# Performance work log

Hardware: AMD Instinct MI355X
Metric: run time of the kernel (lower is better)

Reference implementation:

```python
import jax, jax.numpy as jnp
import numpy as np

DIM = 1024
HEADS = 16
HEAD_DIM = DIM // HEADS
THETA = 10000.0


def _freqs_cis(d, n, theta=THETA):
    # complex rotary frequencies, shape (n, d//2)
    pos = jnp.arange(n, dtype=jnp.float32)
    inv = 1.0 / theta ** (jnp.arange(0, d, 2, dtype=jnp.float32) / d)
    ang = jnp.outer(pos, inv)
    return jax.lax.complex(jnp.cos(ang), jnp.sin(ang))


def _to_complex(x):
    # (..., d) -> (..., d//2) complex via adjacent pairs
    xr = x.astype(jnp.float32).reshape(*x.shape[:-1], -1, 2)
    return jax.lax.complex(xr[..., 0], xr[..., 1])


def _to_real(xc):
    # (..., d//2) complex -> (..., d) interleaved real/imag
    return jnp.stack([jnp.real(xc), jnp.imag(xc)], axis=-1).reshape(*xc.shape[:-1], -1)


def setup_inputs() -> dict:
    key = jax.random.key(0)
    k1, k2, k3 = jax.random.split(key, 3)
    b, seq = 2, 2048
    x = jax.random.normal(k1, (b, DIM, seq), dtype=jnp.float32)
    w_qkv = jax.random.normal(k2, (3 * DIM, DIM), dtype=jnp.float32) * (DIM ** -0.5)
    w_out = jax.random.normal(k3, (DIM, DIM), dtype=jnp.float32) * (DIM ** -0.5)
    return {"x": x, "w_qkv": w_qkv, "w_out": w_out}


def reference(x, w_qkv, w_out):
    b, dim, n = x.shape
    h, hd = HEADS, HEAD_DIM
    scale = hd ** -0.5
    xt = jnp.swapaxes(x, -1, -2)                      # (b, t, dim)
    qkv = jnp.einsum('btd,ed->bte', xt, w_qkv)        # (b, t, 3*dim)
    q, k, v = jnp.split(qkv, 3, axis=-1)
    q = q.reshape(b, n, h, hd)
    k = k.reshape(b, n, h, hd)
    v = v.reshape(b, n, h, hd)
    # rotary embedding on q, k
    fc = _freqs_cis(hd, n)[None, :, None, :]          # (1, t, 1, hd//2)
    q = _to_real(_to_complex(q) * fc).astype(x.dtype)
    k = _to_real(_to_complex(k) * fc).astype(x.dtype)
    # naive full attention
    logits = jnp.einsum('bqhd,bkhd->bhqk', q, k) * scale
    probs = jax.nn.softmax(logits, axis=-1)
    out = jnp.einsum('bhqk,bkhd->bqhd', probs, v)     # (b, t, h, hd)
    out = out.reshape(b, n, dim)
    out = jnp.einsum('btd,ed->bte', out, w_out)       # (b, t, dim)
    return jnp.swapaxes(out, -1, -2)                  # (b, dim, t)
```

## Files before the change

kernel.cpp:

```cpp
#include <hip/hip_runtime.h>
#include <hip/hip_bf16.h>
#include <math.h>

#define B 2
#define N 2048
#define D 1024
#define H 16
#define HD 64

typedef __attribute__((ext_vector_type(8))) short short8;
typedef __attribute__((ext_vector_type(4))) float f32x4;
typedef __attribute__((ext_vector_type(16))) float f32x16;
typedef __attribute__((ext_vector_type(4))) unsigned short ush4;
typedef __attribute__((ext_vector_type(4))) unsigned int uint4v;

__device__ __forceinline__ float bf2f(unsigned short u) {
  unsigned int x = ((unsigned int)u) << 16;
  float f;
  __builtin_memcpy(&f, &x, 4);
  return f;
}
__device__ __forceinline__ unsigned short f2bf(float f) {
  unsigned int x;
  __builtin_memcpy(&x, &f, 4);
  x = x + 0x7fffu + ((x >> 16) & 1u);
  return (unsigned short)(x >> 16);
}
__device__ __forceinline__ unsigned int pk2(float lo, float hi) {
  union { __hip_bfloat162 h; unsigned int u; } cv;
  cv.h = __float22bfloat162_rn(make_float2(lo, hi));
  return cv.u;
}
__device__ __forceinline__ short8 mk_frag(unsigned int w0, unsigned int w1,
                                          unsigned int w2, unsigned int w3) {
  union { uint4v u; short8 s; } cv;
  cv.u = (uint4v){w0, w1, w2, w3};
  return cv.s;
}

__device__ __forceinline__ void gload16(const unsigned short* g, unsigned short* l) {
  __builtin_amdgcn_global_load_lds(
      (const __attribute__((address_space(1))) unsigned int*)(const void*)g,
      (__attribute__((address_space(3))) unsigned int*)(void*)l, 16, 0, 0);
}

__global__ void prep_k(const float* __restrict__ wqkv, unsigned short* __restrict__ wqkv_bf,
                       const float* __restrict__ wout, unsigned short* __restrict__ wout_bf,
                       float2* __restrict__ tab) {
  int blk = blockIdx.x;
  if (blk < 4096) {
    const float* src = (blk < 3072) ? wqkv : wout;
    unsigned short* dst = (blk < 3072) ? wqkv_bf : wout_bf;
    int i = (blk < 3072 ? blk : blk - 3072) * 256 + threadIdx.x;
    float4 v = ((const float4*)src)[i];
    ush4 o;
    o[0] = f2bf(v.x); o[1] = f2bf(v.y); o[2] = f2bf(v.z); o[3] = f2bf(v.w);
    *(ush4*)&dst[i * 4] = o;
  } else {
    int idx = (blk - 4096) * 256 + threadIdx.x;
    int t = idx >> 5, p = idx & 31;
    float inv = powf(10000.f, -(float)p / 32.f);
    float ang = (float)t * inv;
    float s, c;
    sincosf(ang, &s, &c);
    tab[idx] = make_float2(c, s);
  }
}

__global__ __launch_bounds__(256) void transpose_x(const float* __restrict__ x,
                                                   unsigned short* __restrict__ xt) {
  __shared__ float tile[32][33];
  const int tx = threadIdx.x, ty = threadIdx.y;
  const int t0 = blockIdx.x * 32, d0 = blockIdx.y * 32, bb = blockIdx.z;
#pragma unroll
  for (int i = 0; i < 4; ++i) {
    int r = ty * 4 + i;
    tile[r][tx] = x[(size_t)bb * D * N + (size_t)(d0 + r) * N + t0 + tx];
  }
  __syncthreads();
#pragma unroll
  for (int i = 0; i < 4; ++i) {
    int r = ty * 4 + i;
    xt[((size_t)(bb * N) + t0 + r) * D + d0 + tx] = f2bf(tile[tx][r]);
  }
}

template <int MODE>
__global__ __launch_bounds__(256) void gemm_bt(const unsigned short* __restrict__ A,
                                               const unsigned short* __restrict__ Bt,
                                               float* __restrict__ outf,
                                               unsigned short* __restrict__ qkbuf,
                                               unsigned short* __restrict__ vtbuf) {
  __shared__ unsigned short Asm[128 * 64];
  __shared__ unsigned short Bsm[128 * 64];
  const int tid = threadIdx.x;
  const int lane = tid & 63, wid = tid >> 6;
  const int ln = lane & 15, lh = lane >> 4;
  const int wr = wid >> 1, wc = wid & 1;
  const int m0 = blockIdx.x * 128, n0 = blockIdx.y * 128;

  f32x4 acc[4][4];
#pragma unroll
  for (int i = 0; i < 4; ++i)
#pragma unroll
    for (int j = 0; j < 4; ++j) acc[i][j] = (f32x4){0.f, 0.f, 0.f, 0.f};

  for (int k0 = 0; k0 < 1024; k0 += 64) {
#pragma unroll
    for (int jj = 0; jj < 4; ++jj) {
      int slot = tid + jj * 256;
      int row = slot >> 3, u = slot & 7;
      int usw = (u ^ (row & 7)) * 8;
      gload16(&A[(size_t)(m0 + row) * 1024 + k0 + usw], &Asm[slot * 8]);
    }
#pragma unroll
    for (int jj = 0; jj < 4; ++jj) {
      int slot = tid + jj * 256;
      int row = slot >> 3, u = slot & 7;
      int usw = (u ^ (row & 7)) * 8;
      gload16(&Bt[(size_t)(n0 + row) * 1024 + k0 + usw], &Bsm[slot * 8]);
    }
    __syncthreads();
#pragma unroll
    for (int s = 0; s < 2; ++s) {
      short8 af[4], bfr[4];
#pragma unroll
      for (int i = 0; i < 4; ++i) {
        int row = wr * 64 + i * 16 + ln;
        int u = ((s * 4 + lh) ^ (row & 7)) * 8;
        af[i] = *(const short8*)&Asm[row * 64 + u];
      }
#pragma unroll
      for (int j = 0; j < 4; ++j) {
        int row = wc * 64 + j * 16 + ln;
        int u = ((s * 4 + lh) ^ (row & 7)) * 8;
        bfr[j] = *(const short8*)&Bsm[row * 64 + u];
      }
#pragma unroll
      for (int i = 0; i < 4; ++i)
#pragma unroll
        for (int j = 0; j < 4; ++j)
          acc[i][j] = __builtin_amdgcn_mfma_f32_16x16x32_bf16(af[i], bfr[j], acc[i][j], 0, 0, 0);
    }
    __syncthreads();
  }

#pragma unroll
  for (int i = 0; i < 4; ++i) {
    int mrow = m0 + wr * 64 + i * 16 + lh * 4;
    int bb = mrow >> 11, t = mrow & 2047;
#pragma unroll
    for (int j = 0; j < 4; ++j) {
      int e = n0 + wc * 64 + j * 16 + ln;
      if (MODE == 1) {
        float* op = outf + (size_t)bb * D * N + (size_t)e * N + t;
        *(f32x4*)op = acc[i][j];
      } else {
        if (e < 2048) {
#pragma unroll
          for (int jj = 0; jj < 4; ++jj)
            qkbuf[((size_t)(bb * N + t + jj)) * 2048 + e] = f2bf(acc[i][j][jj]);
        } else {
          ush4 v;
#pragma unroll
          for (int jj = 0; jj < 4; ++jj) v[jj] = f2bf(acc[i][j][jj]);
          *(ush4*)&vtbuf[((size_t)bb * 1024 + (e - 2048)) * N + t] = v;
        }
      }
    }
  }
}

__global__ void rope_kernel(unsigned short* __restrict__ qk, const float2* __restrict__ tab) {
  int idx = blockIdx.x * 256 + threadIdx.x;
  int e = (idx & 255) * 8;
  int t = (idx >> 8) & 2047;
  int bb = idx >> 19;
  int p0 = (e & 63) >> 1;
  const float qscl = 0.125f * 1.4426950408889634f;
  float sc = (e < 1024) ? qscl : 1.0f;
  unsigned short* p = qk + ((size_t)(bb * N + t)) * 2048 + e;
  short8 v = *(short8*)p;
#pragma unroll
  for (int q = 0; q < 4; ++q) {
    float2 cs = tab[t * 32 + p0 + q];
    float xe = bf2f((unsigned short)v[2 * q]);
    float xo = bf2f((unsigned short)v[2 * q + 1]);
    v[2 * q] = (short)f2bf((xe * cs.x - xo * cs.y) * sc);
    v[2 * q + 1] = (short)f2bf((xe * cs.y + xo * cs.x) * sc);
  }
  *(short8*)p = v;
}

__global__ __launch_bounds__(512, 4) void attn_kernel(const unsigned short* __restrict__ qk,
                                                      const unsigned short* __restrict__ vt,
                                                      unsigned short* __restrict__ ob) {
  __shared__ __align__(16) char smem[66048];
  const int tid = threadIdx.x;
  const int lane = tid & 63, wid = tid >> 6;
  const int l31 = lane & 31, hi = lane >> 5;
  const int g = wid >> 2, wl = wid & 3;
  const int tidg = tid & 255;
  const int L = blockIdx.x;
  const int hh = L & 31, qb = L >> 5;
  const int bb = hh >> 4, h = hh & 15;
  const unsigned short* Qg = qk + (size_t)bb * N * 2048 + h * 64;
  const unsigned short* Kg = Qg + 1024;
  const unsigned short* Vg = vt + ((size_t)bb * 1024 + h * 64) * N;

  unsigned short* Ksm[2] = {(unsigned short*)smem + (g * 2 + 0) * 4096,
                            (unsigned short*)smem + (g * 2 + 1) * 4096};
  unsigned short* Vsm[2] = {(unsigned short*)(smem + 32768) + (g * 2 + 0) * 4096,
                            (unsigned short*)(smem + 32768) + (g * 2 + 1) * 4096};

  const int q = qb * 128 + wl * 32 + l31;
  short8 qf[4];
#pragma unroll
  for (int c = 0; c < 4; ++c)
    qf[c] = *(const short8*)&Qg[(size_t)q * 2048 + c * 16 + hi * 8];

  f32x16 oL, oH;
#pragma unroll
  for (int r = 0; r < 16; ++r) { oL[r] = 0.f; oH[r] = 0.f; }
  float lrun = 0.f;

  const int kb0 = g * 1024;
  auto STAGE = [&](int buf, int kb) {
#pragma unroll
    for (int jj = 0; jj < 2; ++jj) {
      int slot = tidg + jj * 256;
      int row = slot >> 3, u = slot & 7;
      int usw = (u ^ (row & 7)) * 8;
      gload16(&Kg[(size_t)(kb + row) * 2048 + usw], &Ksm[buf][slot * 8]);
    }
#pragma unroll
    for (int jj = 0; jj < 2; ++jj) {
      int slot = tidg + jj * 256;
      int row = slot >> 3, u = slot & 7;
      int usw = (u ^ (row & 7)) * 8;
      gload16(&Vg[(size_t)row * N + kb + usw], &Vsm[buf][slot * 8]);
    }
  };

  STAGE(0, kb0);
  __syncthreads();
  int cur = 0;
  for (int t = 0; t < 16; ++t) {
    if (t < 15) STAGE(cur ^ 1, kb0 + (t + 1) * 64);
    f32x16 s0, s1;
#pragma unroll
    for (int r = 0; r < 16; ++r) { s0[r] = 0.f; s1[r] = 0.f; }
    __builtin_amdgcn_s_setprio(1);
#pragma unroll
    for (int c = 0; c < 4; ++c) {
      short8 ka = *(const short8*)&Ksm[cur][l31 * 64 + (((c * 2 + hi) ^ (l31 & 7)) * 8)];
      s0 = __builtin_amdgcn_mfma_f32_32x32x16_bf16(ka, qf[c], s0, 0, 0, 0);
      int r1 = 32 + l31;
      short8 kb2 = *(const short8*)&Ksm[cur][r1 * 64 + (((c * 2 + hi) ^ (r1 & 7)) * 8)];
      s1 = __builtin_amdgcn_mfma_f32_32x32x16_bf16(kb2, qf[c], s1, 0, 0, 0);
    }
    __builtin_amdgcn_s_setprio(0);
    float lsum = 0.f;
#pragma unroll
    for (int r = 0; r < 16; ++r) {
      s0[r] = __builtin_amdgcn_exp2f(s0[r]);
      s1[r] = __builtin_amdgcn_exp2f(s1[r]);
      lsum += s0[r] + s1[r];
    }
    lrun += lsum;
    unsigned int W[16];
#pragma unroll
    for (int i = 0; i < 8; ++i) {
      W[i] = pk2(s0[2 * i], s0[2 * i + 1]);
      W[8 + i] = pk2(s1[2 * i], s1[2 * i + 1]);
    }
    short8 pf[4];
#pragma unroll
    for (int c = 0; c < 4; ++c) {
      unsigned int a0 = W[4 * c + 0], b0 = W[4 * c + 2];
      unsigned int a1 = W[4 * c + 1], b1 = W[4 * c + 3];
      asm volatile("v_permlane32_swap_b32 %0, %1" : "+v"(a0), "+v"(b0));
      asm volatile("v_permlane32_swap_b32 %0, %1" : "+v"(a1), "+v"(b1));
      pf[c] = mk_frag(a0, a1, b0, b1);
    }
    __builtin_amdgcn_s_setprio(1);
#pragma unroll
    for (int c = 0; c < 4; ++c) {
      short8 va = *(const short8*)&Vsm[cur][l31 * 64 + (((c * 2 + hi) ^ (l31 & 7)) * 8)];
      oL = __builtin_amdgcn_mfma_f32_32x32x16_bf16(va, pf[c], oL, 0, 0, 0);
      int rH = 32 + l31;
      short8 vb = *(const short8*)&Vsm[cur][rH * 64 + (((c * 2 + hi) ^ (rH & 7)) * 8)];
      oH = __builtin_amdgcn_mfma_f32_32x32x16_bf16(vb, pf[c], oH, 0, 0, 0);
    }
    __builtin_amdgcn_s_setprio(0);
    __syncthreads();
    cur ^= 1;
  }
  lrun += __shfl_xor(lrun, 32, 64);

  __syncthreads();
  float* cmb = (float*)smem;
  float* lbuf = (float*)(smem + 65536);
  const int ql = wl * 32 + l31;
  if (g) {
#pragma unroll
    for (int r4 = 0; r4 < 4; ++r4) {
      int bo = (ql * 256 + r4 * 32 + hi * 16) ^ ((ql & 7) << 4);
      *(f32x4*)((char*)cmb + bo) =
          (f32x4){oL[r4 * 4], oL[r4 * 4 + 1], oL[r4 * 4 + 2], oL[r4 * 4 + 3]};
      int bo2 = (ql * 256 + 128 + r4 * 32 + hi * 16) ^ ((ql & 7) << 4);
      *(f32x4*)((char*)cmb + bo2) =
          (f32x4){oH[r4 * 4], oH[r4 * 4 + 1], oH[r4 * 4 + 2], oH[r4 * 4 + 3]};
    }
    if (!hi) lbuf[ql] = lrun;
  }
  __syncthreads();
  if (!g) {
#pragma unroll
    for (int r4 = 0; r4 < 4; ++r4) {
      int bo = (ql * 256 + r4 * 32 + hi * 16) ^ ((ql & 7) << 4);
      f32x4 pL = *(const f32x4*)((const char*)cmb + bo);
      int bo2 = (ql * 256 + 128 + r4 * 32 + hi * 16) ^ ((ql & 7) << 4);
      f32x4 pH = *(const f32x4*)((const char*)cmb + bo2);
#pragma unroll
      for (int i = 0; i < 4; ++i) {
        oL[r4 * 4 + i] += pL[i];
        oH[r4 * 4 + i] += pH[i];
      }
    }
    lrun += lbuf[ql];
    float inv = 1.f / lrun;
    unsigned short* obp = ob + ((size_t)(bb * N + q)) * 1024 + h * 64;
#pragma unroll
    for (int r4 = 0; r4 < 4; ++r4) {
      ush4 vL, vH;
#pragma unroll
      for (int i = 0; i < 4; ++i) {
        vL[i] = f2bf(oL[r4 * 4 + i] * inv);
        vH[i] = f2bf(oH[r4 * 4 + i] * inv);
      }
      *(ush4*)&obp[r4 * 8 + hi * 4] = vL;
      *(ush4*)&obp[32 + r4 * 8 + hi * 4] = vH;
    }
  }
}

extern "C" void kernel_launch(void* const* d_in, const int* in_sizes, int n_in,
                              void* d_out, int out_size, void* d_ws, size_t ws_size,
                              hipStream_t stream) {
  const float* x = (const float*)d_in[0];
  const float* w_qkv = (const float*)d_in[1];
  const float* w_out = (const float*)d_in[2];
  float* out = (float*)d_out;
  char* ws = (char*)d_ws;

  unsigned short* wqkv_bf = (unsigned short*)ws;
  unsigned short* wout_bf = (unsigned short*)(ws + 6291456);
  unsigned short* xt      = (unsigned short*)(ws + 8388608);
  unsigned short* qkbuf   = (unsigned short*)(ws + 16777216);
  unsigned short* vtbuf   = (unsigned short*)(ws + 33554432);
  float2* tab             = (float2*)(ws + 41943040);

  prep_k<<<4352, 256, 0, stream>>>(w_qkv, wqkv_bf, w_out, wout_bf, tab);
  transpose_x<<<dim3(N / 32, D / 32, B), dim3(32, 8), 0, stream>>>(x, xt);

  gemm_bt<0><<<dim3(32, 24), 256, 0, stream>>>(xt, wqkv_bf, nullptr, qkbuf, vtbuf);
  rope_kernel<<<4096, 256, 0, stream>>>(qkbuf, tab);
  attn_kernel<<<512, 512, 0, stream>>>(qkbuf, vtbuf, xt );
  gemm_bt<1><<<dim3(32, 8), 256, 0, stream>>>(xt, wout_bf, out, nullptr, nullptr);
}
```

Before: 133.4 us.

## Split Q/K buffers, store Q transposed, stage K/V through registers

```diff
diff --git a/kernel.cpp b/kernel.cpp
--- a/kernel.cpp
+++ b/kernel.cpp
@@ -46,7 +46,7 @@
 
 __global__ void prep_k(const float* __restrict__ wqkv, unsigned short* __restrict__ wqkv_bf,
                        const float* __restrict__ wout, unsigned short* __restrict__ wout_bf,
-                       float2* __restrict__ tab) {
+                       float2* __restrict__ tab, float2* __restrict__ tabT) {
   int blk = blockIdx.x;
   if (blk < 4096) {
     const float* src = (blk < 3072) ? wqkv : wout;
@@ -64,6 +64,7 @@
     float s, c;
     sincosf(ang, &s, &c);
     tab[idx] = make_float2(c, s);
+    tabT[p * 2048 + t] = make_float2(c, s);
   }
 }
 
@@ -89,7 +90,8 @@
 __global__ __launch_bounds__(256) void gemm_bt(const unsigned short* __restrict__ A,
                                                const unsigned short* __restrict__ Bt,
                                                float* __restrict__ outf,
-                                               unsigned short* __restrict__ qkbuf,
+                                               unsigned short* __restrict__ q_em,
+                                               unsigned short* __restrict__ kbuf,
                                                unsigned short* __restrict__ vtbuf) {
   __shared__ unsigned short Asm[128 * 64];
   __shared__ unsigned short Bsm[128 * 64];
@@ -156,14 +158,16 @@
         float* op = outf + (size_t)bb * D * N + (size_t)e * N + t;
         *(f32x4*)op = acc[i][j];
       } else {
-        if (e < 2048) {
+        ush4 v;
+#pragma unroll
+        for (int jj = 0; jj < 4; ++jj) v[jj] = f2bf(acc[i][j][jj]);
+        if (e < 1024) {
+          *(ush4*)&q_em[((size_t)bb * 1024 + e) * N + t] = v;
+        } else if (e < 2048) {
 #pragma unroll
           for (int jj = 0; jj < 4; ++jj)
-            qkbuf[((size_t)(bb * N + t + jj)) * 2048 + e] = f2bf(acc[i][j][jj]);
+            kbuf[((size_t)(bb * N + t + jj)) * 1024 + (e - 1024)] = v[jj];
         } else {
-          ush4 v;
-#pragma unroll
-          for (int jj = 0; jj < 4; ++jj) v[jj] = f2bf(acc[i][j][jj]);
           *(ush4*)&vtbuf[((size_t)bb * 1024 + (e - 2048)) * N + t] = v;
         }
       }
@@ -171,28 +175,53 @@
   }
 }
 
-__global__ void rope_kernel(unsigned short* __restrict__ qk, const float2* __restrict__ tab) {
-  int idx = blockIdx.x * 256 + threadIdx.x;
-  int e = (idx & 255) * 8;
-  int t = (idx >> 8) & 2047;
-  int bb = idx >> 19;
-  int p0 = (e & 63) >> 1;
+__global__ void rope2_kernel(unsigned short* __restrict__ q_em,
+                             unsigned short* __restrict__ kbuf,
+                             const float2* __restrict__ tab,
+                             const float2* __restrict__ tabT) {
   const float qscl = 0.125f * 1.4426950408889634f;
-  float sc = (e < 1024) ? qscl : 1.0f;
-  unsigned short* p = qk + ((size_t)(bb * N + t)) * 2048 + e;
-  short8 v = *(short8*)p;
-#pragma unroll
-  for (int q = 0; q < 4; ++q) {
-    float2 cs = tab[t * 32 + p0 + q];
-    float xe = bf2f((unsigned short)v[2 * q]);
-    float xo = bf2f((unsigned short)v[2 * q + 1]);
-    v[2 * q] = (short)f2bf((xe * cs.x - xo * cs.y) * sc);
-    v[2 * q + 1] = (short)f2bf((xe * cs.y + xo * cs.x) * sc);
-  }
-  *(short8*)p = v;
-}
-
-__global__ __launch_bounds__(512, 4) void attn_kernel(const unsigned short* __restrict__ qk,
+  int blk = blockIdx.x;
+  if (blk < 1024) {
+    int idx = blk * 256 + threadIdx.x;
+    int t0 = (idx & 255) * 8;
+    int pr = idx >> 8;
+    int p = pr & 31, h = (pr >> 5) & 15, bb = pr >> 9;
+    unsigned short* re = q_em + ((size_t)bb * 1024 + h * 64 + 2 * p) * N + t0;
+    unsigned short* ro = re + N;
+    short8 ve = *(short8*)re, vo = *(short8*)ro;
+    const float2* ct = &tabT[p * 2048 + t0];
+#pragma unroll
+    for (int i = 0; i < 8; ++i) {
+      float2 cs = ct[i];
+      float xe = bf2f((unsigned short)ve[i]);
+      float xo = bf2f((unsigned short)vo[i]);
+      ve[i] = (short)f2bf((xe * cs.x - xo * cs.y) * qscl);
+      vo[i] = (short)f2bf((xe * cs.y + xo * cs.x) * qscl);
+    }
+    *(short8*)re = ve;
+    *(short8*)ro = vo;
+  } else {
+    int idx = (blk - 1024) * 256 + threadIdx.x;
+    int e = (idx & 127) * 8;
+    int t = (idx >> 7) & 2047;
+    int bb = idx >> 18;
+    int p0 = (e & 63) >> 1;
+    unsigned short* p = kbuf + ((size_t)(bb * N + t)) * 1024 + e;
+    short8 v = *(short8*)p;
+#pragma unroll
+    for (int q = 0; q < 4; ++q) {
+      float2 cs = tab[t * 32 + p0 + q];
+      float xe = bf2f((unsigned short)v[2 * q]);
+      float xo = bf2f((unsigned short)v[2 * q + 1]);
+      v[2 * q] = (short)f2bf(xe * cs.x - xo * cs.y);
+      v[2 * q + 1] = (short)f2bf(xe * cs.y + xo * cs.x);
+    }
+    *(short8*)p = v;
+  }
+}
+
+__global__ __launch_bounds__(512, 4) void attn_kernel(const unsigned short* __restrict__ q_em,
+                                                      const unsigned short* __restrict__ kbuf,
                                                       const unsigned short* __restrict__ vt,
                                                       unsigned short* __restrict__ ob) {
   __shared__ __align__(16) char smem[66048];
@@ -204,20 +233,25 @@
   const int L = blockIdx.x;
   const int hh = L & 31, qb = L >> 5;
   const int bb = hh >> 4, h = hh & 15;
-  const unsigned short* Qg = qk + (size_t)bb * N * 2048 + h * 64;
-  const unsigned short* Kg = Qg + 1024;
+  const unsigned short* Qg = q_em + ((size_t)bb * 1024 + h * 64) * N;
+  const unsigned short* Kg = kbuf + (size_t)bb * N * 1024 + h * 64;
   const unsigned short* Vg = vt + ((size_t)bb * 1024 + h * 64) * N;
 
-  unsigned short* Ksm[2] = {(unsigned short*)smem + (g * 2 + 0) * 4096,
-                            (unsigned short*)smem + (g * 2 + 1) * 4096};
-  unsigned short* Vsm[2] = {(unsigned short*)(smem + 32768) + (g * 2 + 0) * 4096,
-                            (unsigned short*)(smem + 32768) + (g * 2 + 1) * 4096};
+  unsigned short* K0 = (unsigned short*)smem + (g * 2 + 0) * 4096;
+  unsigned short* K1 = (unsigned short*)smem + (g * 2 + 1) * 4096;
+  unsigned short* V0 = (unsigned short*)(smem + 32768) + (g * 2 + 0) * 4096;
+  unsigned short* V1 = (unsigned short*)(smem + 32768) + (g * 2 + 1) * 4096;
 
   const int q = qb * 128 + wl * 32 + l31;
   short8 qf[4];
 #pragma unroll
-  for (int c = 0; c < 4; ++c)
-    qf[c] = *(const short8*)&Qg[(size_t)q * 2048 + c * 16 + hi * 8];
+  for (int c = 0; c < 4; ++c) {
+    short8 f;
+#pragma unroll
+    for (int j = 0; j < 8; ++j)
+      f[j] = (short)Qg[(size_t)(c * 16 + hi * 8 + j) * N + q];
+    qf[c] = f;
+  }
 
   f32x16 oL, oH;
 #pragma unroll
@@ -225,38 +259,34 @@
   float lrun = 0.f;
 
   const int kb0 = g * 1024;
-  auto STAGE = [&](int buf, int kb) {
-#pragma unroll
-    for (int jj = 0; jj < 2; ++jj) {
-      int slot = tidg + jj * 256;
-      int row = slot >> 3, u = slot & 7;
-      int usw = (u ^ (row & 7)) * 8;
-      gload16(&Kg[(size_t)(kb + row) * 2048 + usw], &Ksm[buf][slot * 8]);
-    }
-#pragma unroll
-    for (int jj = 0; jj < 2; ++jj) {
-      int slot = tidg + jj * 256;
-      int row = slot >> 3, u = slot & 7;
-      int usw = (u ^ (row & 7)) * 8;
-      gload16(&Vg[(size_t)row * N + kb + usw], &Vsm[buf][slot * 8]);
-    }
+  const int row0 = tidg >> 3, u0 = tidg & 7;
+  const int usw0 = (u0 ^ (row0 & 7)) * 8;
+  const int usw1 = (u0 ^ ((row0 + 32) & 7)) * 8;
+  uint4v kra, krb, vra, vrb;
+
+  auto LOADNEXT = [&](int kb) {
+    kra = *(const uint4v*)&Kg[(size_t)(kb + row0) * 1024 + u0 * 8];
+    krb = *(const uint4v*)&Kg[(size_t)(kb + row0 + 32) * 1024 + u0 * 8];
+    vra = *(const uint4v*)&Vg[(size_t)row0 * N + kb + u0 * 8];
+    vrb = *(const uint4v*)&Vg[(size_t)(row0 + 32) * N + kb + u0 * 8];
   };
-
-  STAGE(0, kb0);
-  __syncthreads();
-  int cur = 0;
-  for (int t = 0; t < 16; ++t) {
-    if (t < 15) STAGE(cur ^ 1, kb0 + (t + 1) * 64);
+  auto WRITESTAGE = [&](unsigned short* Kb, unsigned short* Vb) {
+    *(uint4v*)&Kb[row0 * 64 + usw0] = kra;
+    *(uint4v*)&Kb[(row0 + 32) * 64 + usw1] = krb;
+    *(uint4v*)&Vb[row0 * 64 + usw0] = vra;
+    *(uint4v*)&Vb[(row0 + 32) * 64 + usw1] = vrb;
+  };
+  auto COMPUTE = [&](const unsigned short* Kb, const unsigned short* Vb) {
     f32x16 s0, s1;
 #pragma unroll
     for (int r = 0; r < 16; ++r) { s0[r] = 0.f; s1[r] = 0.f; }
     __builtin_amdgcn_s_setprio(1);
 #pragma unroll
     for (int c = 0; c < 4; ++c) {
-      short8 ka = *(const short8*)&Ksm[cur][l31 * 64 + (((c * 2 + hi) ^ (l31 & 7)) * 8)];
+      short8 ka = *(const short8*)&Kb[l31 * 64 + (((c * 2 + hi) ^ (l31 & 7)) * 8)];
       s0 = __builtin_amdgcn_mfma_f32_32x32x16_bf16(ka, qf[c], s0, 0, 0, 0);
       int r1 = 32 + l31;
-      short8 kb2 = *(const short8*)&Ksm[cur][r1 * 64 + (((c * 2 + hi) ^ (r1 & 7)) * 8)];
+      short8 kb2 = *(const short8*)&Kb[r1 * 64 + (((c * 2 + hi) ^ (r1 & 7)) * 8)];
       s1 = __builtin_amdgcn_mfma_f32_32x32x16_bf16(kb2, qf[c], s1, 0, 0, 0);
     }
     __builtin_amdgcn_s_setprio(0);
@@ -286,19 +316,30 @@
     __builtin_amdgcn_s_setprio(1);
 #pragma unroll
     for (int c = 0; c < 4; ++c) {
-      short8 va = *(const short8*)&Vsm[cur][l31 * 64 + (((c * 2 + hi) ^ (l31 & 7)) * 8)];
+      short8 va = *(const short8*)&Vb[l31 * 64 + (((c * 2 + hi) ^ (l31 & 7)) * 8)];
       oL = __builtin_amdgcn_mfma_f32_32x32x16_bf16(va, pf[c], oL, 0, 0, 0);
       int rH = 32 + l31;
-      short8 vb = *(const short8*)&Vsm[cur][rH * 64 + (((c * 2 + hi) ^ (rH & 7)) * 8)];
+      short8 vb = *(const short8*)&Vb[rH * 64 + (((c * 2 + hi) ^ (rH & 7)) * 8)];
       oH = __builtin_amdgcn_mfma_f32_32x32x16_bf16(vb, pf[c], oH, 0, 0, 0);
     }
     __builtin_amdgcn_s_setprio(0);
+  };
+
+  LOADNEXT(kb0);
+  WRITESTAGE(K0, V0);
+  __syncthreads();
+  for (int tt = 0; tt < 16; tt += 2) {
+    LOADNEXT(kb0 + (tt + 1) * 64);
+    COMPUTE(K0, V0);
+    WRITESTAGE(K1, V1);
     __syncthreads();
-    cur ^= 1;
+    if (tt + 2 < 16) LOADNEXT(kb0 + (tt + 2) * 64);
+    COMPUTE(K1, V1);
+    if (tt + 2 < 16) WRITESTAGE(K0, V0);
+    __syncthreads();
   }
   lrun += __shfl_xor(lrun, 32, 64);
 
-  __syncthreads();
   float* cmb = (float*)smem;
   float* lbuf = (float*)(smem + 65536);
   const int ql = wl * 32 + l31;
@@ -357,15 +398,17 @@
   unsigned short* wqkv_bf = (unsigned short*)ws;
   unsigned short* wout_bf = (unsigned short*)(ws + 6291456);
   unsigned short* xt      = (unsigned short*)(ws + 8388608);
-  unsigned short* qkbuf   = (unsigned short*)(ws + 16777216);
+  unsigned short* q_em    = (unsigned short*)(ws + 16777216);
+  unsigned short* kbuf    = (unsigned short*)(ws + 25165824);
   unsigned short* vtbuf   = (unsigned short*)(ws + 33554432);
   float2* tab             = (float2*)(ws + 41943040);
-
-  prep_k<<<4352, 256, 0, stream>>>(w_qkv, wqkv_bf, w_out, wout_bf, tab);
+  float2* tabT            = (float2*)(ws + 42467328);
+
+  prep_k<<<4352, 256, 0, stream>>>(w_qkv, wqkv_bf, w_out, wout_bf, tab, tabT);
   transpose_x<<<dim3(N / 32, D / 32, B), dim3(32, 8), 0, stream>>>(x, xt);
 
-  gemm_bt<0><<<dim3(32, 24), 256, 0, stream>>>(xt, wqkv_bf, nullptr, qkbuf, vtbuf);
-  rope_kernel<<<4096, 256, 0, stream>>>(qkbuf, tab);
-  attn_kernel<<<512, 512, 0, stream>>>(qkbuf, vtbuf, xt );
-  gemm_bt<1><<<dim3(32, 8), 256, 0, stream>>>(xt, wout_bf, out, nullptr, nullptr);
-}
+  gemm_bt<0><<<dim3(32, 24), 256, 0, stream>>>(xt, wqkv_bf, nullptr, q_em, kbuf, vtbuf);
+  rope2_kernel<<<3072, 256, 0, stream>>>(q_em, kbuf, tab, tabT);
+  attn_kernel<<<512, 512, 0, stream>>>(q_em, kbuf, vtbuf, xt );
+  gemm_bt<1><<<dim3(32, 8), 256, 0, stream>>>(xt, wout_bf, out, nullptr, nullptr, nullptr);
+}
```

Measured after the change: 185.4 us. +38.9%, slower.
